# Kernel tuning notes

Hardware: AMD Instinct MI355X
Metric: run time of the kernel (lower is better)

Reference implementation:

```python
import jax, jax.numpy as jnp
import numpy as np
import math

VOCAB = 50257
BLOCK = 2048
NE = 768


def setup_inputs() -> dict:
    key = jax.random.key(0)
    ks = jax.random.split(key, 12)
    s = 0.02
    idx = jax.random.randint(ks[0], (4, 2048), 0, VOCAB, dtype=jnp.int64 if jax.config.jax_enable_x64 else jnp.int32)
    tok_emb = jax.random.normal(ks[1], (VOCAB, NE), jnp.float32) * s
    pos_emb = jax.random.normal(ks[2], (BLOCK, NE), jnp.float32) * s
    Wk = jax.random.normal(ks[3], (NE, NE), jnp.float32) * s
    bk = jnp.zeros((NE,), jnp.float32)
    Wq = jax.random.normal(ks[4], (NE, NE), jnp.float32) * s
    bq = jnp.zeros((NE,), jnp.float32)
    Wv = jax.random.normal(ks[5], (NE, NE), jnp.float32) * s
    bv = jnp.zeros((NE,), jnp.float32)
    ln_g = jnp.ones((NE,), jnp.float32)
    ln_b = jnp.zeros((NE,), jnp.float32)
    Wh = jax.random.normal(ks[6], (NE, VOCAB), jnp.float32) * s
    bh = jnp.zeros((VOCAB,), jnp.float32)
    return {"idx": idx, "tok_emb": tok_emb, "pos_emb": pos_emb, "Wq": Wq, "bq": bq,
            "Wk": Wk, "bk": bk, "Wv": Wv, "bv": bv, "ln_g": ln_g, "ln_b": ln_b,
            "Wh": Wh, "bh": bh}


def reference(idx, tok_emb, pos_emb, Wq, bq, Wk, bk, Wv, bv, ln_g, ln_b, Wh, bh):
    B, T = idx.shape
    C = tok_emb.shape[1]
    x = tok_emb[idx] + pos_emb[:T]  # [B,T,C]
    q = jnp.einsum('btc,cd->btd', x, Wq) + bq
    k = jnp.einsum('btc,cd->btd', x, Wk) + bk
    v = jnp.einsum('btc,cd->btd', x, Wv) + bv
    att = jnp.einsum('btd,bsd->bts', q, k) / math.sqrt(C)  # [B,T,T]
    causal = jnp.tril(jnp.ones((T, T), bool))
    att = jnp.where(causal, att, -jnp.inf)
    att = jax.nn.softmax(att, axis=-1)
    y = jnp.einsum('bts,bsd->btd', att, v)
    # LayerNorm (eps=1e-5, torch default)
    mu = jnp.mean(y, axis=-1, keepdims=True)
    var = jnp.mean((y - mu) ** 2, axis=-1, keepdims=True)
    yn = (y - mu) * jax.lax.rsqrt(var + 1e-5) * ln_g + ln_b
    logits = jnp.einsum('btc,cv->btv', yn, Wh) + bh
    return logits
```

## Files before the change

### kernel.cpp

```cpp
#include <hip/hip_runtime.h>
#include <hip/hip_bf16.h>
#include <math.h>

typedef __bf16 bf16x8 __attribute__((ext_vector_type(8)));
typedef float  f32x4  __attribute__((ext_vector_type(4)));

#define GAS(p) ((const __attribute__((address_space(1))) void*)(p))
#define LAS(p) ((__attribute__((address_space(3))) void*)(p))

static constexpr int NE = 768;

__global__ __launch_bounds__(256) void k_embed(const int* __restrict__ idx,
    const float* __restrict__ tok, const float* __restrict__ pos,
    __hip_bfloat16* __restrict__ xb)
{
    int bt = blockIdx.x;
    int t  = bt & 2047;
    int token = idx[bt];
    const float* te = tok + (size_t)token * NE;
    const float* pe = pos + (size_t)t * NE;
    __hip_bfloat16* o = xb + (size_t)bt * NE;
    for (int c = threadIdx.x; c < NE; c += 256)
        o[c] = __float2bfloat16(te[c] + pe[c]);
}

__global__ __launch_bounds__(256) void k_transpose_f32_bf16(
    const float* __restrict__ in, __hip_bfloat16* __restrict__ out,
    int R, int C, int outRows)
{
    __shared__ float tile[32][33];
    int c0 = blockIdx.x * 32, r0 = blockIdx.y * 32;
    int tx = threadIdx.x & 31, ty = threadIdx.x >> 5;
    #pragma unroll
    for (int i = 0; i < 32; i += 8) {
        int r = r0 + ty + i, c = c0 + tx;
        tile[ty + i][tx] = (r < R && c < C) ? in[(size_t)r * C + c] : 0.f;
    }
    __syncthreads();
    #pragma unroll
    for (int i = 0; i < 32; i += 8) {
        int oc = c0 + ty + i, orr = r0 + tx;
        if (oc < outRows && orr < R)
            out[(size_t)oc * R + orr] = __float2bfloat16(tile[tx][ty + i]);
    }
}

__global__ __launch_bounds__(256) void k_transpose_wh(
    const float* __restrict__ in, __hip_bfloat16* __restrict__ out,
    int R , int C )
{
    __shared__ float tile[64][65];
    const int n0 = blockIdx.x * 64, k0 = blockIdx.y * 64;
    const int t = threadIdx.x;
    if (n0 + 64 <= C) {
        #pragma unroll
        for (int pass = 0; pass < 4; ++pass) {
            int idx = pass * 256 + t;
            int kr = idx >> 4, nc4 = (idx & 15) * 4;
            float4 v = *(const float4*)(in + (size_t)(k0 + kr) * C + n0 + nc4);
            tile[kr][nc4] = v.x; tile[kr][nc4 + 1] = v.y;
            tile[kr][nc4 + 2] = v.z; tile[kr][nc4 + 3] = v.w;
        }
    } else {
        #pragma unroll
        for (int pass = 0; pass < 16; ++pass) {
            int idx = pass * 256 + t;
            int kr = idx >> 6, nc = idx & 63;
            int c = n0 + nc;
            tile[kr][nc] = (c < C) ? in[(size_t)(k0 + kr) * C + c] : 0.f;
        }
    }
    __syncthreads();
    #pragma unroll
    for (int pass = 0; pass < 2; ++pass) {
        int nr = pass * 32 + (t >> 3);
        int kc = (t & 7) * 8;
        bf16x8 v;
        #pragma unroll
        for (int j = 0; j < 8; ++j) {
            __hip_bfloat16 h = __float2bfloat16(tile[kc + j][nr]);
            v[j] = *reinterpret_cast<__bf16*>(&h);
        }
        *(bf16x8*)(out + (size_t)(n0 + nr) * R + k0 + kc) = v;
    }
}

__global__ __launch_bounds__(256) void k_transpose_bf16(
    const __hip_bfloat16* __restrict__ in, __hip_bfloat16* __restrict__ out,
    int R, int C)
{
    __shared__ __hip_bfloat16 tile[32][33];
    size_t boff = (size_t)blockIdx.z * R * C;
    int c0 = blockIdx.x * 32, r0 = blockIdx.y * 32;
    int tx = threadIdx.x & 31, ty = threadIdx.x >> 5;
    #pragma unroll
    for (int i = 0; i < 32; i += 8)
        tile[ty + i][tx] = in[boff + (size_t)(r0 + ty + i) * C + (c0 + tx)];
    __syncthreads();
    #pragma unroll
    for (int i = 0; i < 32; i += 8)
        out[boff + (size_t)(c0 + ty + i) * R + (r0 + tx)] = tile[tx][ty + i];
}

__global__ __launch_bounds__(256) void k_pack_bias(const float* __restrict__ bq,
    const float* __restrict__ bk, const float* __restrict__ bv, float* __restrict__ o)
{
    int i = blockIdx.x * 256 + threadIdx.x;
    if (i < 768) o[i] = bq[i];
    else if (i < 1536) o[i] = bk[i - 768];
    else if (i < 2304) o[i] = bv[i - 1536];
}

template<int MODE>
__global__ __launch_bounds__(256) void k_gemm(
    const __hip_bfloat16* __restrict__ A, const __hip_bfloat16* __restrict__ Bt,
    int K, int lda, int ldb,
    size_t strideA, size_t strideB, size_t strideC,
    float* __restrict__ outf, int ldc, int ncols,
    const float* __restrict__ bias, float scale,
    __hip_bfloat16* __restrict__ oq, __hip_bfloat16* __restrict__ ok,
    __hip_bfloat16* __restrict__ ov)
{
    int bn = blockIdx.x, bm = blockIdx.y, bz = blockIdx.z;
    if constexpr (MODE == 2) bm = (int)gridDim.y - 1 - bm;
    __shared__ __align__(16) __hip_bfloat16 As[128 * 32];
    __shared__ __align__(16) __hip_bfloat16 Bs[128 * 32];
    const __hip_bfloat16* Ab = A  + bz * strideA + (size_t)bm * 128 * lda;
    const __hip_bfloat16* Bb = Bt + bz * strideB + (size_t)bn * 128 * ldb;
    int tid = threadIdx.x, w = tid >> 6, lane = tid & 63;
    int wr = w >> 1, wc = w & 1;
    f32x4 acc[4][4] = {};
    int sr = tid >> 2, sc = (tid & 3) * 8;
    int lr = lane & 15, lk = (lane >> 4) * 8;

    const int kend = (MODE == 2) ? (bm + 1) * 128 : K;

    for (int k0 = 0; k0 < kend; k0 += 32) {
        __syncthreads();
        #pragma unroll
        for (int i = 0; i < 2; ++i) {
            __builtin_amdgcn_global_load_lds(GAS(Ab + (size_t)(i * 64 + sr) * lda + k0 + sc),
                                             LAS((char*)As + i * 4096 + w * 1024), 16, 0, 0);
            __builtin_amdgcn_global_load_lds(GAS(Bb + (size_t)(i * 64 + sr) * ldb + k0 + sc),
                                             LAS((char*)Bs + i * 4096 + w * 1024), 16, 0, 0);
        }
        __syncthreads();
        bf16x8 af[4], bfv[4];
        #pragma unroll
        for (int mi = 0; mi < 4; ++mi)
            af[mi] = *(const bf16x8*)(As + (wr * 64 + mi * 16 + lr) * 32 + lk);
        #pragma unroll
        for (int ni = 0; ni < 4; ++ni)
            bfv[ni] = *(const bf16x8*)(Bs + (wc * 64 + ni * 16 + lr) * 32 + lk);
        #pragma unroll
        for (int mi = 0; mi < 4; ++mi)
            #pragma unroll
            for (int ni = 0; ni < 4; ++ni)
                acc[mi][ni] = __builtin_amdgcn_mfma_f32_16x16x32_bf16(af[mi], bfv[ni], acc[mi][ni], 0, 0, 0);
    }

    int r4 = (lane >> 4) * 4;
    #pragma unroll
    for (int mi = 0; mi < 4; ++mi) {
        #pragma unroll
        for (int ni = 0; ni < 4; ++ni) {
            #pragma unroll
            for (int r = 0; r < 4; ++r) {
                int row = bm * 128 + wr * 64 + mi * 16 + r4 + r;
                int col = bn * 128 + wc * 64 + ni * 16 + lr;
                outf[bz * strideC + (size_t)row * ldc + col] = acc[mi][ni][r];
            }
        }
    }
}

template<int MODE>
__global__ __launch_bounds__(512, 2) void k_gemm8(
    const __hip_bfloat16* __restrict__ A, const __hip_bfloat16* __restrict__ Bt,
    float* __restrict__ outf, int ldc, int ncols,
    const float* __restrict__ bias, float scale,
    __hip_bfloat16* __restrict__ oq, __hip_bfloat16* __restrict__ ok,
    __hip_bfloat16* __restrict__ ov,
    size_t strideA, size_t strideB, size_t strideC)
{
    constexpr int K = 768, NT = K / 64, NI = NT / 2;
    __shared__ __align__(16) __hip_bfloat16 As[2][2][128 * 64];
    __shared__ __align__(16) __hip_bfloat16 Bs[2][2][128 * 64];

    const int Nx = (int)gridDim.x;
    const int qq = Nx >> 3, rr = Nx & 7;
    const int xcd = (int)blockIdx.x & 7, xidx = (int)blockIdx.x >> 3;
    const int bn = (xcd < rr ? xcd * (qq + 1) : rr * (qq + 1) + (xcd - rr) * qq) + xidx;
    const int bm = blockIdx.y, bz = blockIdx.z;
    if (MODE == 1 && bn > bm) return;
    const int tid = threadIdx.x;
    const int w = tid >> 6, lane = tid & 63;
    const int wr = w >> 2, wc = w & 3;
    const int lr = lane & 15, lu = lane >> 4;

    const int sr = tid >> 3;
    const int su = (tid & 7) ^ (sr & 7);
    const __hip_bfloat16* Ap = A  + bz * strideA + (size_t)(bm * 256) * K;
    const __hip_bfloat16* Bp = Bt + bz * strideB + (size_t)(bn * 256) * K;

    f32x4 acc[8][4] = {};
    bf16x8 bq[4][2];

    auto stageAh = [&](int t, int h) {
        #pragma unroll
        for (int l = 0; l < 2; ++l)
            __builtin_amdgcn_global_load_lds(
                GAS(Ap + (size_t)(h * 128 + l * 64 + sr) * K + t * 64 + su * 8),
                LAS(&As[t & 1][h][l * 4096 + tid * 8]), 16, 0, 0);
    };
    auto stageBh = [&](int t, int h) {
        #pragma unroll
        for (int l = 0; l < 2; ++l)
            __builtin_amdgcn_global_load_lds(
                GAS(Bp + (size_t)(h * 128 + l * 64 + sr) * K + t * 64 + su * 8),
                LAS(&Bs[t & 1][h][l * 4096 + tid * 8]), 16, 0, 0);
    };
    auto rdA = [&](int b, int q, int f, int kk) {
        int row = q * 32 + f * 16 + lr;
        return *(const bf16x8*)&As[b][wr][row * 64 + (((kk * 4 + lu) ^ (row & 7)) << 3)];
    };
    auto rdB = [&](int b, int n, int kk) {
        int row = (wc & 1) * 64 + n * 16 + lr;
        return *(const bf16x8*)&Bs[b][wc >> 1][row * 64 + (((kk * 4 + lu) ^ (row & 7)) << 3)];
    };

#define BAR() asm volatile("s_barrier" ::: "memory")
#define VM4() asm volatile("s_waitcnt vmcnt(4)" ::: "memory")
#define VM0() asm volatile("s_waitcnt vmcnt(0)" ::: "memory")
#define CLUSTER(Q)                                                                                          \
    __builtin_amdgcn_s_setprio(1);                                                                          \
    _Pragma("unroll") for (int n = 0; n < 4; ++n)                                                           \
        acc[2*(Q)+0][n] = __builtin_amdgcn_mfma_f32_16x16x32_bf16(af[0][0], bq[n][0], acc[2*(Q)+0][n], 0, 0, 0); \
    _Pragma("unroll") for (int n = 0; n < 4; ++n)                                                           \
        acc[2*(Q)+1][n] = __builtin_amdgcn_mfma_f32_16x16x32_bf16(af[1][0], bq[n][0], acc[2*(Q)+1][n], 0, 0, 0); \
    _Pragma("unroll") for (int n = 0; n < 4; ++n)                                                           \
        acc[2*(Q)+0][n] = __builtin_amdgcn_mfma_f32_16x16x32_bf16(af[0][1], bq[n][1], acc[2*(Q)+0][n], 0, 0, 0); \
    _Pragma("unroll") for (int n = 0; n < 4; ++n)                                                           \
        acc[2*(Q)+1][n] = __builtin_amdgcn_mfma_f32_16x16x32_bf16(af[1][1], bq[n][1], acc[2*(Q)+1][n], 0, 0, 0); \
    __builtin_amdgcn_s_setprio(0);
#define PH(B_, Q_, STAGE)                                                       \
    {   bf16x8 af[2][2];                                                        \
        _Pragma("unroll") for (int f = 0; f < 2; ++f) {                         \
            af[f][0] = rdA(B_, Q_, f, 0); af[f][1] = rdA(B_, Q_, f, 1); }       \
        STAGE                                                                   \
        CLUSTER(Q_)                                                             \
        BAR(); }
#define PHV(B_, Q_, STAGE, VMSTMT)                                              \
    {   bf16x8 af[2][2];                                                        \
        _Pragma("unroll") for (int f = 0; f < 2; ++f) {                         \
            af[f][0] = rdA(B_, Q_, f, 0); af[f][1] = rdA(B_, Q_, f, 1); }       \
        STAGE                                                                   \
        VMSTMT                                                                  \
        BAR();                                                                  \
        CLUSTER(Q_)                                                             \
        BAR(); }

    stageBh(0, 0); stageBh(0, 1);
    stageAh(0, 0); stageAh(0, 1);
    stageBh(1, 0); stageBh(1, 1);
    VM4();
    BAR();

    for (int i = 0; i < NI; ++i) {
        const int t0 = 2 * i, t1 = 2 * i + 1;
        const bool full = (i + 1 < NI);
        #pragma unroll
        for (int n = 0; n < 4; ++n) { bq[n][0] = rdB(0, n, 0); bq[n][1] = rdB(0, n, 1); }
        PH(0, 0, { stageAh(t1, 0); stageAh(t1, 1); })
        PH(0, 1, { if (full) stageBh(t0 + 2, 0); })
        PH(0, 2, { if (full) stageBh(t0 + 2, 1); })
        PHV(0, 3, { }, { if (full) { VM4(); } else { VM0(); } })
        #pragma unroll
        for (int n = 0; n < 4; ++n) { bq[n][0] = rdB(1, n, 0); bq[n][1] = rdB(1, n, 1); }
        PH(1, 0, { if (full) stageAh(t0 + 2, 0); })
        PH(1, 1, { if (full) stageAh(t0 + 2, 1); })
        PH(1, 2, { if (full) stageBh(t1 + 2, 0); })
        PHV(1, 3, { if (full) stageBh(t1 + 2, 1); }, { if (full) { VM4(); } else { VM0(); } })
    }
#undef PHV
#undef PH
#undef CLUSTER
#undef VM0
#undef VM4
#undef BAR

    const int r4 = lu * 4;
    #pragma unroll
    for (int m = 0; m < 8; ++m) {
        #pragma unroll
        for (int n = 0; n < 4; ++n) {
            int col = bn * 256 + wc * 64 + n * 16 + lr;
            if constexpr (MODE == 0) {
                float bv_ = bias[col];
                #pragma unroll
                for (int r = 0; r < 4; ++r) {
                    int row = bm * 256 + wr * 128 + m * 16 + r4 + r;
                    __hip_bfloat16 h = __float2bfloat16(acc[m][n][r] + bv_);
                    if (col < 768)       oq[(size_t)row * 768 + col]          = h;
                    else if (col < 1536) ok[(size_t)row * 768 + (col - 768)]  = h;
                    else                 ov[(size_t)row * 768 + (col - 1536)] = h;
                }
            } else if constexpr (MODE == 1) {
                #pragma unroll
                for (int r = 0; r < 4; ++r) {
                    int row = bm * 256 + wr * 128 + m * 16 + r4 + r;
                    outf[bz * strideC + (size_t)row * ldc + col] = acc[m][n][r] * scale;
                }
            } else {
                if (col < ncols) {
                    float bv_ = bias[col];
                    #pragma unroll
                    for (int r = 0; r < 4; ++r) {
                        int row = bm * 256 + wr * 128 + m * 16 + r4 + r;
                        outf[(size_t)row * ldc + col] = acc[m][n][r] + bv_;
                    }
                }
            }
        }
    }
}

__global__ __launch_bounds__(256) void k_softmax(const float* __restrict__ att,
    __hip_bfloat16* __restrict__ P, int T)
{
    int t = blockIdx.x, b = blockIdx.y;
    const float* row = att + ((size_t)b * T + t) * T;
    __hip_bfloat16* prow = P + ((size_t)b * T + t) * T;
    const int n = t + 1;
    const int nz = ((t >> 7) + 1) << 7;
    __shared__ float red[256];
    float4 v[2];
    float mx = -1e30f;
    #pragma unroll
    for (int j = 0; j < 2; ++j) {
        int e = (threadIdx.x + j * 256) * 4;
        v[j] = *(const float4*)(row + e);
        #pragma unroll
        for (int k = 0; k < 4; ++k)
            if (e + k < n) mx = fmaxf(mx, ((const float*)&v[j])[k]);
    }
    red[threadIdx.x] = mx; __syncthreads();
    for (int o = 128; o > 0; o >>= 1) {
        if (threadIdx.x < o) red[threadIdx.x] = fmaxf(red[threadIdx.x], red[threadIdx.x + o]);
        __syncthreads();
    }
    mx = red[0]; __syncthreads();
    float ev[8];
    float sum = 0.f;
    #pragma unroll
    for (int j = 0; j < 2; ++j) {
        int e = (threadIdx.x + j * 256) * 4;
        #pragma unroll
        for (int k = 0; k < 4; ++k) {
            float x = ((const float*)&v[j])[k];
            float ex = (e + k < n) ? __expf(x - mx) : 0.f;
            ev[j * 4 + k] = ex;
            sum += ex;
        }
    }
    red[threadIdx.x] = sum; __syncthreads();
    for (int o = 128; o > 0; o >>= 1) {
        if (threadIdx.x < o) red[threadIdx.x] += red[threadIdx.x + o];
        __syncthreads();
    }
    float inv = 1.f / red[0];
    #pragma unroll
    for (int j = 0; j < 2; ++j) {
        int e = (threadIdx.x + j * 256) * 4;
        #pragma unroll
        for (int k = 0; k < 4; ++k)
            if (e + k < nz) prow[e + k] = __float2bfloat16(ev[j * 4 + k] * inv);
    }
}

__global__ __launch_bounds__(256) void k_layernorm(const float* __restrict__ y,
    const float* __restrict__ g, const float* __restrict__ b,
    __hip_bfloat16* __restrict__ yn)
{
    int row = blockIdx.x;
    const float* yr = y + (size_t)row * NE;
    float s = 0.f, s2 = 0.f;
    for (int c = threadIdx.x; c < NE; c += 256) { float v = yr[c]; s += v; s2 += v * v; }
    __shared__ float r1[256], r2[256];
    r1[threadIdx.x] = s; r2[threadIdx.x] = s2; __syncthreads();
    for (int o = 128; o > 0; o >>= 1) {
        if (threadIdx.x < o) { r1[threadIdx.x] += r1[threadIdx.x + o]; r2[threadIdx.x] += r2[threadIdx.x + o]; }
        __syncthreads();
    }
    float mu = r1[0] / NE;
    float var = r2[0] / NE - mu * mu;
    float rs = rsqrtf(var + 1e-5f);
    __hip_bfloat16* o = yn + (size_t)row * NE;
    for (int c = threadIdx.x; c < NE; c += 256)
        o[c] = __float2bfloat16((yr[c] - mu) * rs * g[c] + b[c]);
}

extern "C" void kernel_launch(void* const* d_in, const int* in_sizes, int n_in,
                              void* d_out, int out_size, void* d_ws, size_t ws_size,
                              hipStream_t stream)
{
    const int*   idx  = (const int*)  d_in[0];
    const float* tok  = (const float*)d_in[1];
    const float* pos  = (const float*)d_in[2];
    const float* Wq   = (const float*)d_in[3];
    const float* bq   = (const float*)d_in[4];
    const float* Wk   = (const float*)d_in[5];
    const float* bk   = (const float*)d_in[6];
    const float* Wv   = (const float*)d_in[7];
    const float* bv   = (const float*)d_in[8];
    const float* ln_g = (const float*)d_in[9];
    const float* ln_b = (const float*)d_in[10];
    const float* Wh   = (const float*)d_in[11];
    const float* bh   = (const float*)d_in[12];
    float* out = (float*)d_out;

    const int B = 4, T = 2048, C = 768, V = 50257, Vp = 50432;

    char* p = (char*)d_ws;
    auto take = [&](size_t bytes) { char* r = p; p += (bytes + 255) & ~(size_t)255; return r; };
    __hip_bfloat16* xb    = (__hip_bfloat16*)take((size_t)B * T * C * 2);
    __hip_bfloat16* wqkvT = (__hip_bfloat16*)take((size_t)3 * C * C * 2);
    float*          bqkv  = (float*)take((size_t)3 * C * 4);
    __hip_bfloat16* qb    = (__hip_bfloat16*)take((size_t)B * T * C * 2);
    __hip_bfloat16* kb    = (__hip_bfloat16*)take((size_t)B * T * C * 2);
    __hip_bfloat16* vb    = (__hip_bfloat16*)take((size_t)B * T * C * 2);
    __hip_bfloat16* vT    = (__hip_bfloat16*)take((size_t)B * T * C * 2);
    float*          att   = (float*)take((size_t)B * T * T * 4);
    __hip_bfloat16* P     = (__hip_bfloat16*)take((size_t)B * T * T * 2);
    float*          y     = (float*)take((size_t)B * T * C * 4);
    __hip_bfloat16* yn    = (__hip_bfloat16*)take((size_t)B * T * C * 2);
    __hip_bfloat16* whT   = (__hip_bfloat16*)att;

    float scale = 1.0f / sqrtf((float)C);

    k_embed<<<dim3(B * T), 256, 0, stream>>>(idx, tok, pos, xb);
    k_transpose_f32_bf16<<<dim3(24, 24), 256, 0, stream>>>(Wq, wqkvT,             C, C, C);
    k_transpose_f32_bf16<<<dim3(24, 24), 256, 0, stream>>>(Wk, wqkvT + C * C,     C, C, C);
    k_transpose_f32_bf16<<<dim3(24, 24), 256, 0, stream>>>(Wv, wqkvT + 2 * C * C, C, C, C);
    k_pack_bias<<<dim3(9), 256, 0, stream>>>(bq, bk, bv, bqkv);

    k_gemm8<0><<<dim3(9, 32, 1), 512, 0, stream>>>(xb, wqkvT, nullptr, 0, 2304,
        bqkv, 1.f, qb, kb, vb, 0, 0, 0);

    k_transpose_bf16<<<dim3(24, 64, B), 256, 0, stream>>>(vb, vT, T, C);

    k_gemm8<1><<<dim3(8, 8, B), 512, 0, stream>>>(qb, kb, att, T, T,
        nullptr, scale, nullptr, nullptr, nullptr,
        (size_t)T * C, (size_t)T * C, (size_t)T * T);

    k_softmax<<<dim3(T, B), 256, 0, stream>>>(att, P, T);

    k_gemm<2><<<dim3(6, 16, B), 256, 0, stream>>>(P, vT, T, T, T,
        (size_t)T * T, (size_t)C * T, (size_t)T * C, y, C, 0, nullptr, 1.f,
        nullptr, nullptr, nullptr);

    k_transpose_wh<<<dim3(Vp / 64, C / 64), 256, 0, stream>>>(Wh, whT, C, V);

    k_layernorm<<<dim3(B * T), 256, 0, stream>>>(y, ln_g, ln_b, yn);

    k_gemm8<3><<<dim3(Vp / 256, 32), 512, 0, stream>>>(yn, whT, out, V, V,
        bh, 1.f, nullptr, nullptr, nullptr, 0, 0, 0);
}
```

Baseline: 1.189 ms.

## Double-buffer causal P·V GEMM with swizzled LDS and K=64 tiles

Replaces the generic single-buffered P·V GEMM with a dedicated kernel. It uses 64-wide K tiles, double-buffered LDS staging through global_load_lds with an XOR swizzle, explicit waitcnt and barrier control, and raised wave priority around the MFMA blocks. The aim is to overlap global loads with MFMA work, cut LDS bank conflicts and halve the number of barriers per K step. LDS use per block rises, and the hand-placed waitcnt counts tie the kernel to this exact load schedule.

```diff
diff --git a/kernel.cpp b/kernel.cpp
--- a/kernel.cpp
+++ b/kernel.cpp
@@ -111,64 +111,100 @@
     else if (i < 2304) o[i] = bv[i - 1536];
 }
 
-template<int MODE>
-__global__ __launch_bounds__(256) void k_gemm(
-    const __hip_bfloat16* __restrict__ A, const __hip_bfloat16* __restrict__ Bt,
-    int K, int lda, int ldb,
-    size_t strideA, size_t strideB, size_t strideC,
-    float* __restrict__ outf, int ldc, int ncols,
-    const float* __restrict__ bias, float scale,
-    __hip_bfloat16* __restrict__ oq, __hip_bfloat16* __restrict__ ok,
-    __hip_bfloat16* __restrict__ ov)
-{
-    int bn = blockIdx.x, bm = blockIdx.y, bz = blockIdx.z;
-    if constexpr (MODE == 2) bm = (int)gridDim.y - 1 - bm;
-    __shared__ __align__(16) __hip_bfloat16 As[128 * 32];
-    __shared__ __align__(16) __hip_bfloat16 Bs[128 * 32];
-    const __hip_bfloat16* Ab = A  + bz * strideA + (size_t)bm * 128 * lda;
-    const __hip_bfloat16* Bb = Bt + bz * strideB + (size_t)bn * 128 * ldb;
-    int tid = threadIdx.x, w = tid >> 6, lane = tid & 63;
-    int wr = w >> 1, wc = w & 1;
+__global__ __launch_bounds__(256, 2) void k_gemm_pv(
+    const __hip_bfloat16* __restrict__ Pm,
+    const __hip_bfloat16* __restrict__ Vt,
+    float* __restrict__ y)
+{
+    constexpr int T = 2048, C = 768;
+    __shared__ __align__(16) __hip_bfloat16 As[2][128 * 64];
+    __shared__ __align__(16) __hip_bfloat16 Bs[2][128 * 64];
+
+    const int bn = blockIdx.x;
+    const int bm = (int)gridDim.y - 1 - (int)blockIdx.y;
+    const int bz = blockIdx.z;
+    const int NT = (bm + 1) * 2;
+    const int tid = threadIdx.x;
+    const int w = tid >> 6, lane = tid & 63;
+    const int wr = w >> 1, wc = w & 1;
+    const int lr = lane & 15, lu = lane >> 4;
+
+    const __hip_bfloat16* Ap = Pm + (size_t)bz * T * T + (size_t)(bm * 128) * T;
+    const __hip_bfloat16* Bp = Vt + (size_t)bz * C * T + (size_t)(bn * 128) * T;
+
     f32x4 acc[4][4] = {};
-    int sr = tid >> 2, sc = (tid & 3) * 8;
-    int lr = lane & 15, lk = (lane >> 4) * 8;
-
-    const int kend = (MODE == 2) ? (bm + 1) * 128 : K;
-
-    for (int k0 = 0; k0 < kend; k0 += 32) {
-        __syncthreads();
-        #pragma unroll
-        for (int i = 0; i < 2; ++i) {
-            __builtin_amdgcn_global_load_lds(GAS(Ab + (size_t)(i * 64 + sr) * lda + k0 + sc),
-                                             LAS((char*)As + i * 4096 + w * 1024), 16, 0, 0);
-            __builtin_amdgcn_global_load_lds(GAS(Bb + (size_t)(i * 64 + sr) * ldb + k0 + sc),
-                                             LAS((char*)Bs + i * 4096 + w * 1024), 16, 0, 0);
-        }
-        __syncthreads();
-        bf16x8 af[4], bfv[4];
-        #pragma unroll
-        for (int mi = 0; mi < 4; ++mi)
-            af[mi] = *(const bf16x8*)(As + (wr * 64 + mi * 16 + lr) * 32 + lk);
-        #pragma unroll
-        for (int ni = 0; ni < 4; ++ni)
-            bfv[ni] = *(const bf16x8*)(Bs + (wc * 64 + ni * 16 + lr) * 32 + lk);
-        #pragma unroll
-        for (int mi = 0; mi < 4; ++mi)
+
+    auto stage = [&](int kt, int pb) {
+        #pragma unroll
+        for (int l = 0; l < 4; ++l) {
+            int v = l * 256 + tid;
+            int row = v >> 3, u = (v & 7) ^ (row & 7);
+            __builtin_amdgcn_global_load_lds(GAS(Ap + (size_t)row * T + kt * 64 + u * 8),
+                                             LAS(&As[pb][v * 8]), 16, 0, 0);
+        }
+        #pragma unroll
+        for (int l = 0; l < 4; ++l) {
+            int v = l * 256 + tid;
+            int row = v >> 3, u = (v & 7) ^ (row & 7);
+            __builtin_amdgcn_global_load_lds(GAS(Bp + (size_t)row * T + kt * 64 + u * 8),
+                                             LAS(&Bs[pb][v * 8]), 16, 0, 0);
+        }
+    };
+    auto rdA = [&](int pb, int m, int kk) {
+        int row = wr * 64 + m * 16 + lr;
+        return *(const bf16x8*)&As[pb][row * 64 + (((kk * 4 + lu) ^ (row & 7)) << 3)];
+    };
+    auto rdB = [&](int pb, int n, int kk) {
+        int row = wc * 64 + n * 16 + lr;
+        return *(const bf16x8*)&Bs[pb][row * 64 + (((kk * 4 + lu) ^ (row & 7)) << 3)];
+    };
+
+    stage(0, 0);
+    stage(1, 1);
+    asm volatile("s_waitcnt vmcnt(8)" ::: "memory");
+    asm volatile("s_barrier" ::: "memory");
+
+    for (int kt = 0; kt < NT; ++kt) {
+        const int p = kt & 1;
+        bf16x8 af[4][2], bfv[4][2];
+        #pragma unroll
+        for (int m = 0; m < 4; ++m) { af[m][0] = rdA(p, m, 0); af[m][1] = rdA(p, m, 1); }
+        #pragma unroll
+        for (int n = 0; n < 4; ++n) { bfv[n][0] = rdB(p, n, 0); bfv[n][1] = rdB(p, n, 1); }
+        asm volatile("s_waitcnt lgkmcnt(0)" ::: "memory");
+        asm volatile("s_barrier" ::: "memory");
+        if (kt + 2 < NT) {
+            stage(kt + 2, p);
+            asm volatile("s_waitcnt vmcnt(8)" ::: "memory");
+        } else if (kt + 1 < NT) {
+            asm volatile("s_waitcnt vmcnt(0)" ::: "memory");
+        }
+        asm volatile("s_barrier" ::: "memory");
+        __builtin_amdgcn_s_setprio(1);
+        #pragma unroll
+        for (int m = 0; m < 4; ++m)
             #pragma unroll
-            for (int ni = 0; ni < 4; ++ni)
-                acc[mi][ni] = __builtin_amdgcn_mfma_f32_16x16x32_bf16(af[mi], bfv[ni], acc[mi][ni], 0, 0, 0);
-    }
-
-    int r4 = (lane >> 4) * 4;
-    #pragma unroll
-    for (int mi = 0; mi < 4; ++mi) {
-        #pragma unroll
-        for (int ni = 0; ni < 4; ++ni) {
+            for (int n = 0; n < 4; ++n)
+                acc[m][n] = __builtin_amdgcn_mfma_f32_16x16x32_bf16(af[m][0], bfv[n][0], acc[m][n], 0, 0, 0);
+        #pragma unroll
+        for (int m = 0; m < 4; ++m)
+            #pragma unroll
+            for (int n = 0; n < 4; ++n)
+                acc[m][n] = __builtin_amdgcn_mfma_f32_16x16x32_bf16(af[m][1], bfv[n][1], acc[m][n], 0, 0, 0);
+        __builtin_amdgcn_s_setprio(0);
+    }
+
+    const int r4 = lu * 4;
+    float* yo = y + (size_t)bz * T * C;
+    #pragma unroll
+    for (int m = 0; m < 4; ++m) {
+        #pragma unroll
+        for (int n = 0; n < 4; ++n) {
+            int col = bn * 128 + wc * 64 + n * 16 + lr;
             #pragma unroll
             for (int r = 0; r < 4; ++r) {
-                int row = bm * 128 + wr * 64 + mi * 16 + r4 + r;
-                int col = bn * 128 + wc * 64 + ni * 16 + lr;
-                outf[bz * strideC + (size_t)row * ldc + col] = acc[mi][ni][r];
+                int row = bm * 128 + wr * 64 + m * 16 + r4 + r;
+                yo[(size_t)row * C + col] = acc[m][n][r];
             }
         }
     }
@@ -455,9 +491,7 @@
 
     k_softmax<<<dim3(T, B), 256, 0, stream>>>(att, P, T);
 
-    k_gemm<2><<<dim3(6, 16, B), 256, 0, stream>>>(P, vT, T, T, T,
-        (size_t)T * T, (size_t)C * T, (size_t)T * C, y, C, 0, nullptr, 1.f,
-        nullptr, nullptr, nullptr);
+    k_gemm_pv<<<dim3(6, 16, B), 256, 0, stream>>>(P, vT, y);
 
     k_transpose_wh<<<dim3(Vp / 64, C / 64), 256, 0, stream>>>(Wh, whT, C, V);
 
```

Result: no change. 1.169 ms (-1.6%).
